# Kernel optimization log

Hardware: AMD Instinct MI355X
Metric: run time of the kernel (lower is better)

## Reference

```python
import jax, jax.numpy as jnp
import numpy as np

H, I = 16, 64
SCALE = 1.0 / (I ** 0.5)

def _rel_shift(x):
    # x: (S, J, B, H) -> Transformer-XL relative shift trick
    S, J, B, Hh = x.shape
    pad = jnp.zeros((S, 1, B, Hh), dtype=x.dtype)
    y = jnp.concatenate([pad, x], axis=1)           # (S, J+1, B, H)
    y = y.reshape(J + 1, S, B, Hh)[1:]              # (J, S, B, H)
    return y.reshape(S, J, B, Hh)

def setup_inputs() -> dict:
    key = jax.random.key(0)
    ks = jax.random.split(key, 10)
    S, P, B, E = 1024, 1024, 4, 1024
    J = P + S
    # causal mask: query s may attend keys j <= P + s; True = blocked
    mask = (jnp.arange(J)[None, :] > (P + jnp.arange(S))[:, None])[..., None]  # (S,J,1) bool
    sc = E ** -0.5
    return {
        "inputMHA": jax.random.normal(ks[0], (S, B, E), jnp.float32),
        "posEmbeddings": jax.random.normal(ks[1], (J, E), jnp.float32),
        "memory": jax.random.normal(ks[2], (P, B, E), jnp.float32),
        "u": jax.random.normal(ks[3], (H, I), jnp.float32) * 0.02,
        "v": jax.random.normal(ks[4], (H, I), jnp.float32) * 0.02,
        "mask": mask,
        "W_kv": jax.random.normal(ks[5], (E, 2 * H * I), jnp.float32) * sc,
        "W_q": jax.random.normal(ks[6], (E, H * I), jnp.float32) * sc,
        "W_p": jax.random.normal(ks[7], (E, H * I), jnp.float32) * sc,
        "W_o": jax.random.normal(ks[8], (H * I, E), jnp.float32) * sc,
        "gamma": jnp.ones((E,), jnp.float32),
        "beta": jnp.zeros((E,), jnp.float32),
    }

def reference(inputMHA, posEmbeddings, memory, u, v, mask, W_kv, W_q, W_p, W_o, gamma, beta):
    S, B, E = inputMHA.shape
    P = memory.shape[0]
    J = P + S
    x = jnp.concatenate([memory, inputMHA], axis=0)          # (J,B,E)
    kv = x @ W_kv                                            # (J,B,2HI)
    keys, values = jnp.split(kv, 2, axis=-1)
    q = (inputMHA @ W_q).reshape(S, B, H, I)                 # (S,B,H,I)
    K = keys.reshape(J, B, H, I)
    content = jnp.einsum('sbhi,jbhi->sjbh', q + u, K)        # content score
    p = (posEmbeddings @ W_p).reshape(J, H, I)               # (J,H,I)
    pos = jnp.einsum('sbhi,jhi->sjbh', q + v, p)             # position score
    pos = _rel_shift(pos)
    attn = content + pos                                     # (S,J,B,H)
    attn = jnp.where(mask[..., None], -jnp.inf, attn)        # mask (S,J,1)->(S,J,1,1)
    attn = jax.nn.softmax(attn * jnp.asarray(SCALE, attn.dtype), axis=1)
    V = values.reshape(J, B, H, I)
    awv = jnp.einsum('sjbh,jbhi->sbhi', attn, V).reshape(S, B, H * I)
    out = inputMHA + awv @ W_o                               # residual (dropout = eval identity)
    mean = jnp.mean(out, axis=-1, keepdims=True)
    var = jnp.var(out, axis=-1, keepdims=True)
    return (out - mean) / jnp.sqrt(var + 1e-5) * gamma + beta
```

## Files before the change

### kernel.cpp

```cpp
#include <hip/hip_runtime.h>
#include <hip/hip_bf16.h>

#define S_ 1024
#define P_ 1024
#define B_ 4
#define E_ 1024
#define J_ 2048
#define H_ 16
#define I_ 64

typedef __bf16 bf16_t;
typedef __bf16 bf16x8 __attribute__((ext_vector_type(8)));
typedef __bf16 bf16x4 __attribute__((ext_vector_type(4)));
typedef unsigned short u16x8 __attribute__((ext_vector_type(8)));
typedef float f32x4 __attribute__((ext_vector_type(4)));

#define MFMA16(a, b, c) __builtin_amdgcn_mfma_f32_16x16x32_bf16(a, b, c, 0, 0, 0)

#define SWZ(r, c) (((r) << 6) + ((((((c) >> 3)) ^ ((r) & 7)) << 3)) + ((c) & 7))

__device__ __forceinline__ void g2l16(const bf16_t* g, bf16_t* l) {
    __builtin_amdgcn_global_load_lds(
        (const __attribute__((address_space(1))) unsigned int*)(const void*)g,
        (__attribute__((address_space(3))) unsigned int*)(void*)l,
        16, 0, 0);
}

__global__ __launch_bounds__(256) void prep_kernel(
    const float* __restrict__ memory, const float* __restrict__ input,
    const float* __restrict__ posEmb, bf16_t* __restrict__ Xbf, bf16_t* __restrict__ Pemb,
    const float* __restrict__ W_kv, bf16_t* __restrict__ Wkvt,
    const float* __restrict__ W_q, bf16_t* __restrict__ Wqt,
    const float* __restrict__ W_p, bf16_t* __restrict__ Wpt,
    const float* __restrict__ W_o, bf16_t* __restrict__ Wot) {
    __shared__ float tile[32][33];
    int blk = blockIdx.x;
    int tid = threadIdx.x;
    if (blk < 10240) {
        const float* src;
        bf16_t* dst;
        if (blk < 4096) { src = memory; dst = Xbf; }
        else if (blk < 8192) { blk -= 4096; src = input; dst = Xbf + (size_t)P_ * B_ * E_; }
        else { blk -= 8192; src = posEmb; dst = Pemb; }
        int i = (blk * 256 + tid) * 4;
        float4 v = *(const float4*)(src + i);
        bf16x4 o = {(bf16_t)v.x, (bf16_t)v.y, (bf16_t)v.z, (bf16_t)v.w};
        *(bf16x4*)(dst + i) = o;
        return;
    }
    int t = blk - 10240;
    const float* W;
    bf16_t* Wt;
    int N, xt, yt;
    if (t < 2048) {
        W = W_kv; Wt = Wkvt; N = 2048; xt = t & 63; yt = t >> 6;
    } else {
        int t2 = t - 2048;
        int z = t2 >> 10;
        int rem = t2 & 1023;
        W = (z == 0) ? W_q : (z == 1) ? W_p : W_o;
        Wt = (z == 0) ? Wqt : (z == 1) ? Wpt : Wot;
        N = 1024; xt = rem & 31; yt = rem >> 5;
    }
    int n0 = xt * 32, k0 = yt * 32;
    int x = tid & 31, y = tid >> 5;
    for (int i = 0; i < 32; i += 8)
        tile[y + i][x] = W[(size_t)(k0 + y + i) * N + n0 + x];
    __syncthreads();
    for (int i = 0; i < 32; i += 8)
        Wt[(size_t)(n0 + y + i) * 1024 + k0 + x] = (bf16_t)tile[x][y + i];
}

__device__ __forceinline__ void gemm_tile(
    const bf16_t* __restrict__ A, const bf16_t* __restrict__ Bt, int N,
    int m0, int n0, int epi,
    bf16_t* __restrict__ out0, bf16_t* __restrict__ out1,
    const float* __restrict__ add0, const float* __restrict__ add1,
    float* __restrict__ outf,
    bf16_t* AlL, bf16_t* BlL) {
    const int K = 1024;
    int tid = threadIdx.x;
    int wave = tid >> 6, lane = tid & 63, quad = lane >> 4, l16 = lane & 15;
    int wm = (wave & 1) * 64, wn = (wave >> 1) * 64;
    int lrow = lane >> 3;
    int gsw = ((lane & 7) ^ lrow) << 3;
    f32x4 zero = {0.f, 0.f, 0.f, 0.f};
    f32x4 acc[4][4];
    #pragma unroll
    for (int i = 0; i < 4; i++)
        #pragma unroll
        for (int j = 0; j < 4; j++) acc[i][j] = zero;

    for (int k0 = 0; k0 < K; k0 += 64) {
        __syncthreads();
        #pragma unroll
        for (int r = 0; r < 4; r++) {
            int row0 = r * 32 + wave * 8;
            g2l16(&A[(size_t)(m0 + row0 + lrow) * K + k0 + gsw], &AlL[row0 * 64]);
            g2l16(&Bt[(size_t)(n0 + row0 + lrow) * K + k0 + gsw], &BlL[row0 * 64]);
        }
        __syncthreads();
        #pragma unroll
        for (int ks = 0; ks < 2; ks++) {
            bf16x8 af[4], bfr[4];
            #pragma unroll
            for (int i = 0; i < 4; i++)
                af[i] = *(const bf16x8*)&AlL[SWZ(wm + i * 16 + l16, ks * 32 + quad * 8)];
            #pragma unroll
            for (int j = 0; j < 4; j++)
                bfr[j] = *(const bf16x8*)&BlL[SWZ(wn + j * 16 + l16, ks * 32 + quad * 8)];
            #pragma unroll
            for (int i = 0; i < 4; i++)
                #pragma unroll
                for (int j = 0; j < 4; j++) acc[i][j] = MFMA16(af[i], bfr[j], acc[i][j]);
        }
    }
    #pragma unroll
    for (int i = 0; i < 4; i++)
        #pragma unroll
        for (int j = 0; j < 4; j++)
            #pragma unroll
            for (int reg = 0; reg < 4; reg++) {
                int m = m0 + wm + i * 16 + quad * 4 + reg;
                int n = n0 + wn + j * 16 + l16;
                float v = acc[i][j][reg];
                if (epi == 0) {
                    out0[(size_t)m * N + n] = (bf16_t)v;
                } else if (epi == 1) {
                    out0[(size_t)m * N + n] = (bf16_t)(v + add0[n]);
                    out1[(size_t)m * N + n] = (bf16_t)(v + add1[n]);
                } else {
                    outf[(size_t)m * N + n] = v + add0[(size_t)m * N + n];
                }
            }
}

__global__ __launch_bounds__(256) void gemm3_kernel(
    const bf16_t* __restrict__ Xbf, const bf16_t* __restrict__ Wkvt, bf16_t* __restrict__ kvb,
    const bf16_t* __restrict__ Wqt, bf16_t* __restrict__ qub, bf16_t* __restrict__ qvb,
    const float* __restrict__ u, const float* __restrict__ v,
    const bf16_t* __restrict__ Pemb, const bf16_t* __restrict__ Wpt, bf16_t* __restrict__ pb) {
    __shared__ __attribute__((aligned(16))) bf16_t Al[128 * 64];
    __shared__ __attribute__((aligned(16))) bf16_t Bl[128 * 64];
    int id = blockIdx.x;
    if (id < 1024) {
        int xcd = id & 7, s = id >> 3;
        int m = xcd * 8 + (s & 7), n = s >> 3;
        gemm_tile(Xbf, Wkvt, 2048, m * 128, n * 128, 0,
                  kvb, nullptr, nullptr, nullptr, nullptr, Al, Bl);
    } else if (id < 1280) {
        int t = id - 1024;
        int xcd = t & 7, s = t >> 3;
        int m = xcd * 4 + (s & 3), n = s >> 2;
        gemm_tile(Xbf + (size_t)P_ * B_ * E_, Wqt, 1024, m * 128, n * 128, 1,
                  qub, qvb, u, v, nullptr, Al, Bl);
    } else {
        int t = id - 1280;
        int xcd = t & 7, s = t >> 3;
        int m = xcd * 2 + (s & 1), n = s >> 1;
        gemm_tile(Pemb, Wpt, 1024, m * 128, n * 128, 0,
                  pb, nullptr, nullptr, nullptr, nullptr, Al, Bl);
    }
}

__global__ __launch_bounds__(256) void gemmo_kernel(
    const bf16_t* __restrict__ awvb, const bf16_t* __restrict__ Wot,
    const float* __restrict__ inputMHA, float* __restrict__ opre) {
    __shared__ __attribute__((aligned(16))) bf16_t Al[128 * 64];
    __shared__ __attribute__((aligned(16))) bf16_t Bl[128 * 64];
    int id = blockIdx.x;
    int xcd = id & 7, s = id >> 3;
    int m = xcd * 4 + (s & 3), n = s >> 2;
    gemm_tile(awvb, Wot, 1024, m * 128, n * 128, 2,
              nullptr, nullptr, inputMHA, nullptr, opre, Al, Bl);
}

__global__ __launch_bounds__(256) void flash_kernel(
    const bf16_t* __restrict__ qu, const bf16_t* __restrict__ qv,
    const bf16_t* __restrict__ kv, const bf16_t* __restrict__ pm,
    bf16_t* __restrict__ awv) {
    __shared__ __attribute__((aligned(16))) bf16_t Klds[64 * 64];
    __shared__ __attribute__((aligned(16))) bf16_t Vt[64 * 64];
    __shared__ __attribute__((aligned(16))) bf16_t Plds[128 * 64];
    __shared__ __attribute__((aligned(16))) bf16_t Prob[4 * 16 * 64];

    int tid = threadIdx.x;
    int wave = tid >> 6, lane = tid & 63, quad = lane >> 4, l16 = lane & 15;

    int linear = blockIdx.x;
    int xcd = linear & 7;
    int p = linear >> 3;
    int bh = xcd * 8 + ((p >> 2) & 7);
    int q4 = ((p >> 5) << 2) | (p & 3);
    int s_blk = (q4 < 8) ? q4 : 23 - q4;
    int nt = 17 + s_blk;
    int t0 = 0;
    int t1 = nt;

    int s0 = s_blk * 64;
    int b = bh >> 4, h = bh & 15;
    int srow0 = s0 + wave * 16;

    const bf16_t* qub = qu + ((size_t)(srow0 + l16) * B_ + b) * 1024 + h * 64 + quad * 8;
    const bf16_t* qvb = qv + ((size_t)(srow0 + l16) * B_ + b) * 1024 + h * 64 + quad * 8;
    bf16x8 aqu0 = *(const bf16x8*)(qub);
    bf16x8 aqu1 = *(const bf16x8*)(qub + 32);
    bf16x8 aqv0 = *(const bf16x8*)(qvb);
    bf16x8 aqv1 = *(const bf16x8*)(qvb + 32);

    f32x4 zero = {0.f, 0.f, 0.f, 0.f};
    f32x4 accO[4];
    #pragma unroll
    for (int ot = 0; ot < 4; ot++) accO[ot] = zero;
    float lrowp[4] = {0.f, 0.f, 0.f, 0.f};

    const int w0u = 960 - s0;
    const int woff = 48 - wave * 16;
    const float SCL = 0.125f * 1.44269504088896f;

    int jr = tid >> 3, seg8g = tid & 7;
    int jp = tid & 31, iseg = tid >> 5;
    uint* VtU = (uint*)&Vt[0];
    bf16_t* ProbW = Prob + (wave << 10);

    {
        int j0 = t0 * 64;
        const bf16_t* kp = kv + ((size_t)(j0 + jr) * B_ + b) * 2048 + h * 64 + seg8g * 8;
        uint4 ka = *(const uint4*)kp;
        uint4 kb = *(const uint4*)(kp + (size_t)32 * B_ * 2048);
        const bf16_t* vp = kv + ((size_t)(j0 + jp * 2) * B_ + b) * 2048 + 1024 + h * 64 + iseg * 8;
        u16x8 va = *(const u16x8*)vp;
        u16x8 vb = *(const u16x8*)(vp + (size_t)B_ * 2048);
        uint4 pd[4];
        #pragma unroll
        for (int r = 0; r < 4; r++) {
            int idx = tid + 256 * r;
            int pr = idx >> 3, pg = idx & 7;
            int lr = w0u + j0 + pr; if (lr > J_ - 1) lr = J_ - 1;
            pd[r] = *(const uint4*)(pm + (size_t)lr * 1024 + h * 64 + pg * 8);
        }
        *(uint4*)&Klds[SWZ(jr, seg8g * 8)] = ka;
        *(uint4*)&Klds[SWZ(jr + 32, seg8g * 8)] = kb;
        #pragma unroll
        for (int e = 0; e < 8; e++) {
            int row = iseg * 8 + e;
            VtU[(row << 5) + ((((jp >> 2) ^ (row & 7)) << 2)) + (jp & 3)] =
                (uint)va[e] | ((uint)vb[e] << 16);
        }
        #pragma unroll
        for (int r = 0; r < 4; r++) {
            int idx = tid + 256 * r;
            int pr = idx >> 3, pg = idx & 7;
            *(uint4*)&Plds[SWZ((w0u + j0 + pr) & 127, pg * 8)] = pd[r];
        }
    }
    __syncthreads();

    for (int it = t0; it < t1; it++) {
        int j0 = it * 64;
        bool pf = (it + 1 < t1);
        uint4 ka, kb, pd0, pd1;
        u16x8 va, vb;
        int pr0 = tid >> 3, pg0 = tid & 7;
        int pr1 = (tid + 256) >> 3, pg1 = tid & 7;
        if (pf) {
            int j1 = j0 + 64;
            const bf16_t* kp = kv + ((size_t)(j1 + jr) * B_ + b) * 2048 + h * 64 + seg8g * 8;
            ka = *(const uint4*)kp;
            kb = *(const uint4*)(kp + (size_t)32 * B_ * 2048);
            const bf16_t* vp = kv + ((size_t)(j1 + jp * 2) * B_ + b) * 2048 + 1024 + h * 64 + iseg * 8;
            va = *(const u16x8*)vp;
            vb = *(const u16x8*)(vp + (size_t)B_ * 2048);
            int lr0 = w0u + j0 + 128 + pr0; if (lr0 > J_ - 1) lr0 = J_ - 1;
            int lr1 = w0u + j0 + 128 + pr1; if (lr1 > J_ - 1) lr1 = J_ - 1;
            pd0 = *(const uint4*)(pm + (size_t)lr0 * 1024 + h * 64 + pg0 * 8);
            pd1 = *(const uint4*)(pm + (size_t)lr1 * 1024 + h * 64 + pg1 * 8);
        }

        f32x4 cs[4];
        #pragma unroll
        for (int t = 0; t < 4; t++) cs[t] = zero;
        __builtin_amdgcn_s_setprio(1);
        #pragma unroll
        for (int ks = 0; ks < 2; ks++) {
            bf16x8 aq = ks ? aqu1 : aqu0;
            #pragma unroll
            for (int t = 0; t < 4; t++) {
                bf16x8 bk = *(const bf16x8*)&Klds[SWZ(t * 16 + l16, ks * 32 + quad * 8)];
                cs[t] = MFMA16(aq, bk, cs[t]);
            }
        }
        f32x4 ep[5];
        #pragma unroll
        for (int t = 0; t < 5; t++) ep[t] = zero;
        #pragma unroll
        for (int ks = 0; ks < 2; ks++) {
            bf16x8 aq = ks ? aqv1 : aqv0;
            #pragma unroll
            for (int t = 0; t < 5; t++) {
                int prow = (w0u + j0 + woff + t * 16 + l16) & 127;
                bf16x8 bp = *(const bf16x8*)&Plds[SWZ(prow, ks * 32 + quad * 8)];
                ep[t] = MFMA16(aq, bp, ep[t]);
            }
        }
        __builtin_amdgcn_s_setprio(0);

        #pragma unroll
        for (int reg = 0; reg < 4; reg++) {
            int r = quad * 4 + reg;
            int s = srow0 + r;
            int idx = l16 + 15 - r;
            int srcl = quad * 16 + (idx & 15);
            float sh[5];
            #pragma unroll
            for (int t = 0; t < 5; t++) sh[t] = __shfl(ep[t][reg], srcl);
            float psum = 0.f;
            #pragma unroll
            for (int t = 0; t < 4; t++) {
                float pos = (idx < 16) ? sh[t] : sh[t + 1];
                float p2 = exp2f((cs[t][reg] + pos) * SCL);
                p2 = (j0 + t * 16 + l16 > P_ + s) ? 0.f : p2;
                ProbW[SWZ(r, t * 16 + l16)] = (bf16_t)p2;
                psum += p2;
            }
            lrowp[reg] += psum;
        }

        __builtin_amdgcn_s_setprio(1);
        #pragma unroll
        for (int ks = 0; ks < 2; ks++) {
            bf16x8 pa = *(const bf16x8*)&Prob[(wave << 10) + SWZ(l16, ks * 32 + quad * 8)];
            #pragma unroll
            for (int ot = 0; ot < 4; ot++) {
                bf16x8 bv = *(const bf16x8*)&Vt[SWZ(ot * 16 + l16, ks * 32 + quad * 8)];
                accO[ot] = MFMA16(pa, bv, accO[ot]);
            }
        }
        __builtin_amdgcn_s_setprio(0);

        __syncthreads();
        if (pf) {
            *(uint4*)&Klds[SWZ(jr, seg8g * 8)] = ka;
            *(uint4*)&Klds[SWZ(jr + 32, seg8g * 8)] = kb;
            #pragma unroll
            for (int e2 = 0; e2 < 8; e2++) {
                int row = iseg * 8 + e2;
                VtU[(row << 5) + ((((jp >> 2) ^ (row & 7)) << 2)) + (jp & 3)] =
                    (uint)va[e2] | ((uint)vb[e2] << 16);
            }
            *(uint4*)&Plds[SWZ((w0u + j0 + pr0) & 127, pg0 * 8)] = pd0;
            *(uint4*)&Plds[SWZ((w0u + j0 + pr1) & 127, pg1 * 8)] = pd1;
        }
        __syncthreads();
    }

    #pragma unroll
    for (int reg = 0; reg < 4; reg++) {
        int r = quad * 4 + reg;
        int srow = srow0 + r;
        float l = lrowp[reg];
        #pragma unroll
        for (int d = 1; d < 16; d <<= 1) l += __shfl_xor(l, d);
        float inv = 1.0f / l;
        size_t rowoff = ((size_t)srow * B_ + b) * 1024 + h * 64;
        #pragma unroll
        for (int ot = 0; ot < 4; ot++)
            awv[rowoff + ot * 16 + l16] = (bf16_t)(accO[ot][reg] * inv);
    }
}

__global__ __launch_bounds__(256) void ln_kernel(const float* __restrict__ x,
                                                 const float* __restrict__ gamma,
                                                 const float* __restrict__ beta,
                                                 float* __restrict__ out) {
    int row = blockIdx.x, tid = threadIdx.x;
    int lane = tid & 63, wave = tid >> 6;
    float4 v = ((const float4*)(x + (size_t)row * 1024))[tid];
    float s = v.x + v.y + v.z + v.w;
    float ss = v.x * v.x + v.y * v.y + v.z * v.z + v.w * v.w;
    #pragma unroll
    for (int sh = 1; sh < 64; sh <<= 1) { s += __shfl_xor(s, sh); ss += __shfl_xor(ss, sh); }
    __shared__ float red[8];
    if (lane == 0) { red[wave] = s; red[4 + wave] = ss; }
    __syncthreads();
    s = red[0] + red[1] + red[2] + red[3];
    ss = red[4] + red[5] + red[6] + red[7];
    float mean = s * (1.f / 1024.f);
    float var = ss * (1.f / 1024.f) - mean * mean;
    float inv = rsqrtf(var + 1e-5f);
    float4 g = ((const float4*)gamma)[tid];
    float4 bt = ((const float4*)beta)[tid];
    float4 o;
    o.x = (v.x - mean) * inv * g.x + bt.x;
    o.y = (v.y - mean) * inv * g.y + bt.y;
    o.z = (v.z - mean) * inv * g.z + bt.z;
    o.w = (v.w - mean) * inv * g.w + bt.w;
    ((float4*)(out + (size_t)row * 1024))[tid] = o;
}

extern "C" void kernel_launch(void* const* d_in, const int* in_sizes, int n_in,
                              void* d_out, int out_size, void* d_ws, size_t ws_size,
                              hipStream_t stream) {
    const float* inputMHA = (const float*)d_in[0];
    const float* posEmb   = (const float*)d_in[1];
    const float* memory   = (const float*)d_in[2];
    const float* u        = (const float*)d_in[3];
    const float* v        = (const float*)d_in[4];
    const float* W_kv     = (const float*)d_in[6];
    const float* W_q      = (const float*)d_in[7];
    const float* W_p      = (const float*)d_in[8];
    const float* W_o      = (const float*)d_in[9];
    const float* gamma    = (const float*)d_in[10];
    const float* beta     = (const float*)d_in[11];
    float* out = (float*)d_out;

    char* ws = (char*)d_ws;
    size_t off = 0;
    auto alloc = [&](size_t bytes) -> void* {
        void* p = ws + off;
        off += (bytes + 255) & ~(size_t)255;
        return p;
    };
    bf16_t* Xbf  = (bf16_t*)alloc((size_t)J_ * B_ * E_ * 2);
    bf16_t* Wkvt = (bf16_t*)alloc((size_t)2048 * 1024 * 2);
    bf16_t* Wqt  = (bf16_t*)alloc((size_t)1024 * 1024 * 2);
    bf16_t* Wpt  = (bf16_t*)alloc((size_t)1024 * 1024 * 2);
    bf16_t* Wot  = (bf16_t*)alloc((size_t)1024 * 1024 * 2);
    bf16_t* Pemb = (bf16_t*)alloc((size_t)2048 * 1024 * 2);
    bf16_t* kvb  = (bf16_t*)alloc((size_t)8192 * 2048 * 2);
    bf16_t* qub  = (bf16_t*)alloc((size_t)4096 * 1024 * 2);
    bf16_t* qvb  = (bf16_t*)alloc((size_t)4096 * 1024 * 2);
    bf16_t* pb   = (bf16_t*)alloc((size_t)2048 * 1024 * 2);
    bf16_t* awvb = (bf16_t*)alloc((size_t)4096 * 1024 * 2);
    float*  opre = (float*)alloc((size_t)4096 * 1024 * 4);

    prep_kernel<<<15360, 256, 0, stream>>>(memory, inputMHA, posEmb, Xbf, Pemb,
                                           W_kv, Wkvt, W_q, Wqt, W_p, Wpt, W_o, Wot);

    gemm3_kernel<<<1408, 256, 0, stream>>>(Xbf, Wkvt, kvb, Wqt, qub, qvb, u, v, Pemb, Wpt, pb);

    flash_kernel<<<1024, 256, 0, stream>>>(qub, qvb, kvb, pb, awvb);

    gemmo_kernel<<<256, 256, 0, stream>>>(awvb, Wot, inputMHA, opre);
    ln_kernel<<<S_ * B_, 256, 0, stream>>>(opre, gamma, beta, out);
}
```

Measured before the change: 379.3 us.

## Enlarge flash attention query tile to 128 rows with 8-wave blocks

The flash kernel now processes 128 query rows per block with 8 waves (512 threads) instead of 64 rows with 4 waves, halving the grid. Each K/V/positional tile loaded into LDS is shared by twice as many query rows, reducing global loads per unit of work. The positional ring buffer grows to 256 rows and the block-to-(bh, s) mapping and load-balancing pairing are reworked. The cost is more LDS per block and fewer blocks, which lowers occupancy and coarsens the causal work imbalance.

```diff
diff --git a/kernel.cpp b/kernel.cpp
--- a/kernel.cpp
+++ b/kernel.cpp
@@ -175,29 +175,28 @@
               nullptr, nullptr, inputMHA, nullptr, opre, Al, Bl);
 }
 
-__global__ __launch_bounds__(256) void flash_kernel(
+__global__ __launch_bounds__(512) void flash_kernel(
     const bf16_t* __restrict__ qu, const bf16_t* __restrict__ qv,
     const bf16_t* __restrict__ kv, const bf16_t* __restrict__ pm,
     bf16_t* __restrict__ awv) {
     __shared__ __attribute__((aligned(16))) bf16_t Klds[64 * 64];
     __shared__ __attribute__((aligned(16))) bf16_t Vt[64 * 64];
-    __shared__ __attribute__((aligned(16))) bf16_t Plds[128 * 64];
-    __shared__ __attribute__((aligned(16))) bf16_t Prob[4 * 16 * 64];
+    __shared__ __attribute__((aligned(16))) bf16_t Plds[256 * 64];
+    __shared__ __attribute__((aligned(16))) bf16_t Prob[8 * 16 * 64];
 
     int tid = threadIdx.x;
     int wave = tid >> 6, lane = tid & 63, quad = lane >> 4, l16 = lane & 15;
 
     int linear = blockIdx.x;
     int xcd = linear & 7;
-    int p = linear >> 3;
-    int bh = xcd * 8 + ((p >> 2) & 7);
-    int q4 = ((p >> 5) << 2) | (p & 3);
-    int s_blk = (q4 < 8) ? q4 : 23 - q4;
-    int nt = 17 + s_blk;
-    int t0 = 0;
-    int t1 = nt;
-
-    int s0 = s_blk * 64;
+    int p2 = linear >> 3;
+    int r5 = p2 & 31;
+    int bh = xcd * 8 + (r5 >> 2);
+    int sq = r5 & 3;
+    int s128 = (p2 < 32) ? sq : 7 - sq;
+    int nt = 18 + 2 * s128;
+
+    int s0 = s128 * 128;
     int b = bh >> 4, h = bh & 15;
     int srow0 = s0 + wave * 16;
 
@@ -214,67 +213,67 @@
     for (int ot = 0; ot < 4; ot++) accO[ot] = zero;
     float lrowp[4] = {0.f, 0.f, 0.f, 0.f};
 
-    const int w0u = 960 - s0;
-    const int woff = 48 - wave * 16;
+    const int wb = 896 - s0;
+    const int rdo = 1008 - s0 - wave * 16;
     const float SCL = 0.125f * 1.44269504088896f;
 
     int jr = tid >> 3, seg8g = tid & 7;
-    int jp = tid & 31, iseg = tid >> 5;
+    int jp = tid & 31, iseg = (tid >> 5) & 7;
     uint* VtU = (uint*)&Vt[0];
     bf16_t* ProbW = Prob + (wave << 10);
 
     {
-        int j0 = t0 * 64;
-        const bf16_t* kp = kv + ((size_t)(j0 + jr) * B_ + b) * 2048 + h * 64 + seg8g * 8;
+        const bf16_t* kp = kv + ((size_t)jr * B_ + b) * 2048 + h * 64 + seg8g * 8;
         uint4 ka = *(const uint4*)kp;
-        uint4 kb = *(const uint4*)(kp + (size_t)32 * B_ * 2048);
-        const bf16_t* vp = kv + ((size_t)(j0 + jp * 2) * B_ + b) * 2048 + 1024 + h * 64 + iseg * 8;
-        u16x8 va = *(const u16x8*)vp;
-        u16x8 vb = *(const u16x8*)(vp + (size_t)B_ * 2048);
-        uint4 pd[4];
-        #pragma unroll
-        for (int r = 0; r < 4; r++) {
-            int idx = tid + 256 * r;
+        u16x8 va, vb;
+        if (tid < 256) {
+            const bf16_t* vp = kv + ((size_t)(jp * 2) * B_ + b) * 2048 + 1024 + h * 64 + iseg * 8;
+            va = *(const u16x8*)vp;
+            vb = *(const u16x8*)(vp + (size_t)B_ * 2048);
+        }
+        uint4 pd[3];
+        #pragma unroll
+        for (int r = 0; r < 3; r++) {
+            int idx = tid + 512 * r;
             int pr = idx >> 3, pg = idx & 7;
-            int lr = w0u + j0 + pr; if (lr > J_ - 1) lr = J_ - 1;
+            int lr = wb + pr;
             pd[r] = *(const uint4*)(pm + (size_t)lr * 1024 + h * 64 + pg * 8);
         }
         *(uint4*)&Klds[SWZ(jr, seg8g * 8)] = ka;
-        *(uint4*)&Klds[SWZ(jr + 32, seg8g * 8)] = kb;
-        #pragma unroll
-        for (int e = 0; e < 8; e++) {
-            int row = iseg * 8 + e;
-            VtU[(row << 5) + ((((jp >> 2) ^ (row & 7)) << 2)) + (jp & 3)] =
-                (uint)va[e] | ((uint)vb[e] << 16);
-        }
-        #pragma unroll
-        for (int r = 0; r < 4; r++) {
-            int idx = tid + 256 * r;
+        if (tid < 256) {
+            #pragma unroll
+            for (int e = 0; e < 8; e++) {
+                int row = iseg * 8 + e;
+                VtU[(row << 5) + ((((jp >> 2) ^ (row & 7)) << 2)) + (jp & 3)] =
+                    (uint)va[e] | ((uint)vb[e] << 16);
+            }
+        }
+        #pragma unroll
+        for (int r = 0; r < 3; r++) {
+            int idx = tid + 512 * r;
             int pr = idx >> 3, pg = idx & 7;
-            *(uint4*)&Plds[SWZ((w0u + j0 + pr) & 127, pg * 8)] = pd[r];
+            *(uint4*)&Plds[SWZ((wb + pr) & 255, pg * 8)] = pd[r];
         }
     }
     __syncthreads();
 
-    for (int it = t0; it < t1; it++) {
+    for (int it = 0; it < nt; it++) {
         int j0 = it * 64;
-        bool pf = (it + 1 < t1);
-        uint4 ka, kb, pd0, pd1;
+        bool pf = (it + 1 < nt);
+        uint4 ka, pd0;
         u16x8 va, vb;
         int pr0 = tid >> 3, pg0 = tid & 7;
-        int pr1 = (tid + 256) >> 3, pg1 = tid & 7;
         if (pf) {
             int j1 = j0 + 64;
             const bf16_t* kp = kv + ((size_t)(j1 + jr) * B_ + b) * 2048 + h * 64 + seg8g * 8;
             ka = *(const uint4*)kp;
-            kb = *(const uint4*)(kp + (size_t)32 * B_ * 2048);
-            const bf16_t* vp = kv + ((size_t)(j1 + jp * 2) * B_ + b) * 2048 + 1024 + h * 64 + iseg * 8;
-            va = *(const u16x8*)vp;
-            vb = *(const u16x8*)(vp + (size_t)B_ * 2048);
-            int lr0 = w0u + j0 + 128 + pr0; if (lr0 > J_ - 1) lr0 = J_ - 1;
-            int lr1 = w0u + j0 + 128 + pr1; if (lr1 > J_ - 1) lr1 = J_ - 1;
+            if (tid < 256) {
+                const bf16_t* vp = kv + ((size_t)(j1 + jp * 2) * B_ + b) * 2048 + 1024 + h * 64 + iseg * 8;
+                va = *(const u16x8*)vp;
+                vb = *(const u16x8*)(vp + (size_t)B_ * 2048);
+            }
+            int lr0 = wb + j0 + 192 + pr0; if (lr0 > J_ - 1) lr0 = J_ - 1;
             pd0 = *(const uint4*)(pm + (size_t)lr0 * 1024 + h * 64 + pg0 * 8);
-            pd1 = *(const uint4*)(pm + (size_t)lr1 * 1024 + h * 64 + pg1 * 8);
         }
 
         f32x4 cs[4];
@@ -298,7 +297,7 @@
             bf16x8 aq = ks ? aqv1 : aqv0;
             #pragma unroll
             for (int t = 0; t < 5; t++) {
-                int prow = (w0u + j0 + woff + t * 16 + l16) & 127;
+                int prow = (rdo + j0 + t * 16 + l16) & 255;
                 bf16x8 bp = *(const bf16x8*)&Plds[SWZ(prow, ks * 32 + quad * 8)];
                 ep[t] = MFMA16(aq, bp, ep[t]);
             }
@@ -318,10 +317,10 @@
             #pragma unroll
             for (int t = 0; t < 4; t++) {
                 float pos = (idx < 16) ? sh[t] : sh[t + 1];
-                float p2 = exp2f((cs[t][reg] + pos) * SCL);
-                p2 = (j0 + t * 16 + l16 > P_ + s) ? 0.f : p2;
-                ProbW[SWZ(r, t * 16 + l16)] = (bf16_t)p2;
-                psum += p2;
+                float p2v = exp2f((cs[t][reg] + pos) * SCL);
+                p2v = (j0 + t * 16 + l16 > P_ + s) ? 0.f : p2v;
+                ProbW[SWZ(r, t * 16 + l16)] = (bf16_t)p2v;
+                psum += p2v;
             }
             lrowp[reg] += psum;
         }
@@ -341,15 +340,15 @@
         __syncthreads();
         if (pf) {
             *(uint4*)&Klds[SWZ(jr, seg8g * 8)] = ka;
-            *(uint4*)&Klds[SWZ(jr + 32, seg8g * 8)] = kb;
-            #pragma unroll
-            for (int e2 = 0; e2 < 8; e2++) {
-                int row = iseg * 8 + e2;
-                VtU[(row << 5) + ((((jp >> 2) ^ (row & 7)) << 2)) + (jp & 3)] =
-                    (uint)va[e2] | ((uint)vb[e2] << 16);
-            }
-            *(uint4*)&Plds[SWZ((w0u + j0 + pr0) & 127, pg0 * 8)] = pd0;
-            *(uint4*)&Plds[SWZ((w0u + j0 + pr1) & 127, pg1 * 8)] = pd1;
+            if (tid < 256) {
+                #pragma unroll
+                for (int e2 = 0; e2 < 8; e2++) {
+                    int row = iseg * 8 + e2;
+                    VtU[(row << 5) + ((((jp >> 2) ^ (row & 7)) << 2)) + (jp & 3)] =
+                        (uint)va[e2] | ((uint)vb[e2] << 16);
+                }
+            }
+            *(uint4*)&Plds[SWZ((wb + j0 + 192 + pr0) & 255, pg0 * 8)] = pd0;
         }
         __syncthreads();
     }
@@ -439,7 +438,7 @@
 
     gemm3_kernel<<<1408, 256, 0, stream>>>(Xbf, Wkvt, kvb, Wqt, qub, qvb, u, v, Pemb, Wpt, pb);
 
-    flash_kernel<<<1024, 256, 0, stream>>>(qub, qvb, kvb, pb, awvb);
+    flash_kernel<<<512, 512, 0, stream>>>(qub, qvb, kvb, pb, awvb);
 
     gemmo_kernel<<<256, 256, 0, stream>>>(awvb, Wot, inputMHA, opre);
     ln_kernel<<<S_ * B_, 256, 0, stream>>>(opre, gamma, beta, out);
```

Result: slower. 390.3 us (+2.9%).

## Split flash attention key range in two halves and combine partial outputs

Applied to the files above, without the earlier changes.

Each (query block, batch-head) work item is split into two blocks, each covering half of the key tiles, which doubles the flash kernel grid. Each half writes unnormalised fp32 partial outputs and row sums to a workspace. A new combine kernel adds the two halves, divides by the summed denominator and writes bf16 for the output projection. This is meant to raise parallelism and even out work across CUs. In exchange it adds a large fp32 round trip through memory and one more kernel launch, and the query fragments are loaded twice.

```diff
diff --git a/kernel.cpp b/kernel.cpp
--- a/kernel.cpp
+++ b/kernel.cpp
@@ -178,7 +178,7 @@
 __global__ __launch_bounds__(256) void flash_kernel(
     const bf16_t* __restrict__ qu, const bf16_t* __restrict__ qv,
     const bf16_t* __restrict__ kv, const bf16_t* __restrict__ pm,
-    bf16_t* __restrict__ awv) {
+    float* __restrict__ Oa, float* __restrict__ la) {
     __shared__ __attribute__((aligned(16))) bf16_t Klds[64 * 64];
     __shared__ __attribute__((aligned(16))) bf16_t Vt[64 * 64];
     __shared__ __attribute__((aligned(16))) bf16_t Plds[128 * 64];
@@ -191,11 +191,13 @@
     int xcd = linear & 7;
     int p = linear >> 3;
     int bh = xcd * 8 + ((p >> 2) & 7);
-    int q4 = ((p >> 5) << 2) | (p & 3);
-    int s_blk = (q4 < 8) ? q4 : 23 - q4;
+    int th = ((p >> 5) << 2) | (p & 3);
+    int s_blk = th & 15;
+    int half = th >> 4;
     int nt = 17 + s_blk;
-    int t0 = 0;
-    int t1 = nt;
+    int mid = nt >> 1;
+    int t0 = half ? mid : 0;
+    int t1 = half ? nt : mid;
 
     int s0 = s_blk * 64;
     int b = bh >> 4, h = bh & 15;
@@ -318,10 +320,10 @@
             #pragma unroll
             for (int t = 0; t < 4; t++) {
                 float pos = (idx < 16) ? sh[t] : sh[t + 1];
-                float p2 = exp2f((cs[t][reg] + pos) * SCL);
-                p2 = (j0 + t * 16 + l16 > P_ + s) ? 0.f : p2;
-                ProbW[SWZ(r, t * 16 + l16)] = (bf16_t)p2;
-                psum += p2;
+                float p2v = exp2f((cs[t][reg] + pos) * SCL);
+                p2v = (j0 + t * 16 + l16 > P_ + s) ? 0.f : p2v;
+                ProbW[SWZ(r, t * 16 + l16)] = (bf16_t)p2v;
+                psum += p2v;
             }
             lrowp[reg] += psum;
         }
@@ -354,6 +356,8 @@
         __syncthreads();
     }
 
+    size_t obase = (size_t)half * ((size_t)4096 * 1024);
+    size_t lbase = (size_t)half * ((size_t)S_ * B_ * H_);
     #pragma unroll
     for (int reg = 0; reg < 4; reg++) {
         int r = quad * 4 + reg;
@@ -361,12 +365,26 @@
         float l = lrowp[reg];
         #pragma unroll
         for (int d = 1; d < 16; d <<= 1) l += __shfl_xor(l, d);
-        float inv = 1.0f / l;
+        if (l16 == 0) la[lbase + ((size_t)srow * B_ + b) * H_ + h] = l;
         size_t rowoff = ((size_t)srow * B_ + b) * 1024 + h * 64;
         #pragma unroll
         for (int ot = 0; ot < 4; ot++)
-            awv[rowoff + ot * 16 + l16] = (bf16_t)(accO[ot][reg] * inv);
-    }
+            Oa[obase + rowoff + ot * 16 + l16] = accO[ot][reg];
+    }
+}
+
+__global__ __launch_bounds__(256) void comb_kernel(const float* __restrict__ Oa,
+                                                   const float* __restrict__ la,
+                                                   bf16_t* __restrict__ awv) {
+    int i4 = (blockIdx.x * 256 + threadIdx.x) * 4;
+    int row16 = i4 >> 6;
+    float l = la[row16] + la[(size_t)S_ * B_ * H_ + row16];
+    float inv = 1.0f / l;
+    float4 o0 = *(const float4*)(Oa + i4);
+    float4 o1 = *(const float4*)(Oa + (size_t)4096 * 1024 + i4);
+    bf16x4 r = {(bf16_t)((o0.x + o1.x) * inv), (bf16_t)((o0.y + o1.y) * inv),
+                (bf16_t)((o0.z + o1.z) * inv), (bf16_t)((o0.w + o1.w) * inv)};
+    *(bf16x4*)(awv + i4) = r;
 }
 
 __global__ __launch_bounds__(256) void ln_kernel(const float* __restrict__ x,
@@ -433,13 +451,16 @@
     bf16_t* pb   = (bf16_t*)alloc((size_t)2048 * 1024 * 2);
     bf16_t* awvb = (bf16_t*)alloc((size_t)4096 * 1024 * 2);
     float*  opre = (float*)alloc((size_t)4096 * 1024 * 4);
+    float*  Oa   = (float*)alloc((size_t)2 * 4096 * 1024 * 4);
+    float*  la   = (float*)alloc((size_t)2 * S_ * B_ * H_ * 4);
 
     prep_kernel<<<15360, 256, 0, stream>>>(memory, inputMHA, posEmb, Xbf, Pemb,
                                            W_kv, Wkvt, W_q, Wqt, W_p, Wpt, W_o, Wot);
 
     gemm3_kernel<<<1408, 256, 0, stream>>>(Xbf, Wkvt, kvb, Wqt, qub, qvb, u, v, Pemb, Wpt, pb);
 
-    flash_kernel<<<1024, 256, 0, stream>>>(qub, qvb, kvb, pb, awvb);
+    flash_kernel<<<2048, 256, 0, stream>>>(qub, qvb, kvb, pb, Oa, la);
+    comb_kernel<<<4096, 256, 0, stream>>>(Oa, la, awvb);
 
     gemmo_kernel<<<256, 256, 0, stream>>>(awvb, Wot, inputMHA, opre);
     ln_kernel<<<S_ * B_, 256, 0, stream>>>(opre, gamma, beta, out);
```

New measurement: 396.1 us. +4.4%, slower.
